# Performance work log

Measured on AMD Instinct MI355X. Metric: run time of the kernel, lower is better.

## Reference

```python
import jax, jax.numpy as jnp
import numpy as np

HEAD_SIZE = 128
LAMBDA_INIT = 0.8
FILL = 1e-09  # the module fills masked positions with 1e-9 (not -inf); reproduce faithfully


def setup_inputs() -> dict:
    key = jax.random.key(0)
    ks = jax.random.split(key, 12)
    B, T, C = 8, 2048, 1024
    q = jax.random.normal(ks[0], (B, T, C), dtype=jnp.float32)
    k = jax.random.normal(ks[1], (B, T, C), dtype=jnp.float32)
    v = jax.random.normal(ks[2], (B, T, C), dtype=jnp.float32)
    pad_mask = jax.random.randint(ks[3], (B, T), 0, 2, dtype=jnp.int32)
    scale = 1.0 / np.sqrt(C)
    Wq = jax.random.normal(ks[4], (C, 2 * HEAD_SIZE), dtype=jnp.float32) * scale
    Wk = jax.random.normal(ks[5], (C, 2 * HEAD_SIZE), dtype=jnp.float32) * scale
    Wv = jax.random.normal(ks[6], (C, HEAD_SIZE), dtype=jnp.float32) * scale
    lq1 = jax.random.normal(ks[7], (HEAD_SIZE,), dtype=jnp.float32)
    lk1 = jax.random.normal(ks[8], (HEAD_SIZE,), dtype=jnp.float32)
    lq2 = jax.random.normal(ks[9], (HEAD_SIZE,), dtype=jnp.float32)
    lk2 = jax.random.normal(ks[10], (HEAD_SIZE,), dtype=jnp.float32)
    return {"q": q, "k": k, "v": v, "pad_mask": pad_mask,
            "Wq": Wq, "Wk": Wk, "Wv": Wv,
            "lq1": lq1, "lk1": lk1, "lq2": lq2, "lk2": lk2}


def reference(q, k, v, pad_mask, Wq, Wk, Wv, lq1, lk1, lq2, lk2):
    B, T_q, C = q.shape
    T_k = k.shape[1]
    Q = q @ Wq                      # [B, Tq, 2*hs]
    K = k @ Wk                      # [B, Tk, 2*hs]
    V = v @ Wv                      # [B, Tk, ho]
    Q1, Q2 = jnp.split(Q, 2, axis=-1)
    K1, K2 = jnp.split(K, 2, axis=-1)
    s1 = jnp.einsum("bqd,bkd->bqk", Q1, K1)
    s2 = jnp.einsum("bqd,bkd->bqk", Q2, K2)
    # causal mask: tril(ones, diagonal=1) == 0 -> fill (note diagonal=1, one lookahead)
    causal_fill = jnp.tril(jnp.ones((T_q, T_k), dtype=bool), 1) == False
    s1 = jnp.where(causal_fill[None], FILL, s1)
    s2 = jnp.where(causal_fill[None], FILL, s2)
    # pad mask broadcast over the KEY axis per query row (as in original)
    pad_fill = (pad_mask == 1)[:, :, None]  # [B, Tq, 1]
    s1 = jnp.where(pad_fill, FILL, s1)
    s2 = jnp.where(pad_fill, FILL, s2)
    scale = HEAD_SIZE ** (-0.5)
    lbd = jnp.exp(jnp.dot(lq1, lk1)) - jnp.exp(jnp.dot(lq2, lk2)) + LAMBDA_INIT
    attn = jax.nn.softmax(s1 * scale, axis=-1) - lbd * jax.nn.softmax(s2 * scale, axis=-1)
    return attn @ V                 # [B, Tq, ho]
```

## Files before the change

kernel.cpp:

```cpp
#include <hip/hip_runtime.h>
#include <math.h>


#define T_SEQ 2048
#define NB 8
#define CDIM 1024
#define HS 128

constexpr float SCALE = 0.08838834764831845f;

typedef float f32x4 __attribute__((ext_vector_type(4)));
typedef __bf16 bf16x8 __attribute__((ext_vector_type(8)));
typedef unsigned int u32;

#define MFMA16 __builtin_amdgcn_mfma_f32_16x16x32_bf16

__device__ __forceinline__ void gld16(const void* g, void* l) {
  __builtin_amdgcn_global_load_lds(
      (const __attribute__((address_space(1))) u32*)g,
      (__attribute__((address_space(3))) u32*)l, 16, 0, 0);
}

__device__ __forceinline__ bf16x8 cvt8(f32x4 lo, f32x4 hi) {
  bf16x8 r;
  r[0] = (__bf16)lo.x; r[1] = (__bf16)lo.y; r[2] = (__bf16)lo.z; r[3] = (__bf16)lo.w;
  r[4] = (__bf16)hi.x; r[5] = (__bf16)hi.y; r[6] = (__bf16)hi.z; r[7] = (__bf16)hi.w;
  return r;
}

__global__ __launch_bounds__(128) void lambda_kernel(
    const float* __restrict__ lq1, const float* __restrict__ lk1,
    const float* __restrict__ lq2, const float* __restrict__ lk2,
    float* __restrict__ lbd) {
  __shared__ float r1[128], r2[128];
  int t = threadIdx.x;
  r1[t] = lq1[t] * lk1[t];
  r2[t] = lq2[t] * lk2[t];
  __syncthreads();
  for (int s = 64; s > 0; s >>= 1) {
    if (t < s) { r1[t] += r1[t + s]; r2[t] += r2[t + s]; }
    __syncthreads();
  }
  if (t == 0) *lbd = expf(r1[0]) - expf(r2[0]) + 0.8f;
}

__global__ __launch_bounds__(256) void pack_w(
    const float* __restrict__ Wq, const float* __restrict__ Wk,
    const float* __restrict__ Wv, __bf16* __restrict__ Wp) {
  int nt = blockIdx.x;
  const float* W; int colbase, N;
  if (nt < 16)      { W = Wq; colbase = nt * 16;        N = 256; }
  else if (nt < 32) { W = Wk; colbase = (nt - 16) * 16; N = 256; }
  else              { W = Wv; colbase = (nt - 32) * 16; N = 128; }
  int tid = threadIdx.x;
#pragma unroll
  for (int i = 0; i < 8; ++i) {
    int u = tid + 256 * i;
    int ks = u >> 6, lane = u & 63;
    int l15 = lane & 15, quad = lane >> 4;
    bf16x8 pk;
#pragma unroll
    for (int j = 0; j < 8; ++j)
      pk[j] = (__bf16)W[(size_t)(ks * 32 + quad * 8 + j) * N + colbase + l15];
    *(bf16x8*)(Wp + ((size_t)(nt * 32 + ks) * 64 + lane) * 8) = pk;
  }
}

template<int NT, int NTG>
__device__ __forceinline__ void proj_body(
    const float* __restrict__ Ablk, const __bf16* __restrict__ Wp,
    __bf16* __restrict__ outp, __bf16* __restrict__ Vt,
    int rows0, char* smem) {
  float*  sA = (float*)smem;
  __bf16* sB = (__bf16*)(smem + 32768);
  const int tid = threadIdx.x;
  const int lane = tid & 63, wave = tid >> 6;
  const int l15 = lane & 15, quad = lane >> 4;
  const int arow = lane >> 3;
  const int ac16 = (lane & 7) ^ arow;

  f32x4 acc0[NT], acc1[NT];
#pragma unroll
  for (int j = 0; j < NT; ++j) {
    acc0[j] = (f32x4){0.f, 0.f, 0.f, 0.f};
    acc1[j] = (f32x4){0.f, 0.f, 0.f, 0.f};
  }

  auto stage_ks = [&](int ks, int buf) {
    const float* gA = Ablk + ks * 32;
    float* lA = sA + buf * 4096;
#pragma unroll
    for (int i = 0; i < 4; ++i) {
      int li = wave * 4 + i;
      gld16(gA + (size_t)(li * 8 + arow) * CDIM + ac16 * 4, lA + li * 256);
    }
    __bf16* lB = sB + buf * 8192;
#pragma unroll
    for (int i = 0; i < 4; ++i) {
      int ntl = wave * 4 + i;
      if (ntl < NT)
        gld16(Wp + ((size_t)((NTG + ntl) * 32 + ks) * 64 + lane) * 8,
              lB + ntl * 512);
    }
  };

  stage_ks(0, 0);
  for (int ks = 0; ks < 32; ++ks) {
    const int buf = ks & 1;
    __syncthreads();
    const float* lA = sA + buf * 4096;
    int r0 = wave * 32 + l15;
    f32x4 lo0 = *(const f32x4*)(lA + r0 * 32 + (((quad * 2)     ^ (l15 & 7)) * 4));
    f32x4 hi0 = *(const f32x4*)(lA + r0 * 32 + (((quad * 2 + 1) ^ (l15 & 7)) * 4));
    bf16x8 af0 = cvt8(lo0, hi0);
    int r1 = r0 + 16;
    f32x4 lo1 = *(const f32x4*)(lA + r1 * 32 + (((quad * 2)     ^ (l15 & 7)) * 4));
    f32x4 hi1 = *(const f32x4*)(lA + r1 * 32 + (((quad * 2 + 1) ^ (l15 & 7)) * 4));
    bf16x8 af1 = cvt8(lo1, hi1);
    if (ks < 31) stage_ks(ks + 1, buf ^ 1);
    const __bf16* lB = sB + buf * 8192;
#pragma unroll
    for (int nt = 0; nt < NT; ++nt) {
      bf16x8 bf = *(const bf16x8*)(lB + nt * 512 + lane * 8);
      acc0[nt] = MFMA16(af0, bf, acc0[nt], 0, 0, 0);
      acc1[nt] = MFMA16(af1, bf, acc1[nt], 0, 0, 0);
    }
  }

  __syncthreads();
  __bf16* tile = (__bf16*)smem;
  constexpr int N = NT * 16;
#pragma unroll
  for (int half = 0; half < (NT >> 3); ++half) {
#pragma unroll
    for (int ntl = 0; ntl < 8; ++ntl) {
      f32x4 a0 = acc0[half * 8 + ntl];
      f32x4 a1 = acc1[half * 8 + ntl];
#pragma unroll
      for (int r = 0; r < 4; ++r) {
        tile[(wave * 32 + quad * 4 + r) * 136 + ntl * 16 + l15] = (__bf16)a0[r];
        tile[(wave * 32 + 16 + quad * 4 + r) * 136 + ntl * 16 + l15] = (__bf16)a1[r];
      }
    }
    __syncthreads();
#pragma unroll
    for (int i = 0; i < 8; ++i) {
      int u = tid + 256 * i;
      int row = u >> 4, c8 = u & 15;
      bf16x8 val = *(const bf16x8*)(tile + row * 136 + c8 * 8);
      *(bf16x8*)(outp + (size_t)(rows0 + row) * N + half * 128 + c8 * 8) = val;
    }
    if constexpr (NT == 8) {
      int b = rows0 >> 11, t0 = rows0 & 2047;
#pragma unroll
      for (int i = 0; i < 8; ++i) {
        int u = tid + 256 * i;
        int tc = u & 15, c = u >> 4;
        bf16x8 pk;
#pragma unroll
        for (int j = 0; j < 8; ++j) pk[j] = tile[(tc * 8 + j) * 136 + c];
        *(bf16x8*)(Vt + ((size_t)(b * 128 + c)) * T_SEQ + t0 + tc * 8) = pk;
      }
    }
    __syncthreads();
  }
}

__global__ __launch_bounds__(256, 2) void proj_mfma(
    const float* __restrict__ qin, const float* __restrict__ kin,
    const float* __restrict__ vin, const __bf16* __restrict__ Wp,
    __bf16* __restrict__ Qo, __bf16* __restrict__ Ko,
    __bf16* __restrict__ Vo, __bf16* __restrict__ Vt) {
  __shared__ char smem[65536];
  const int blk = blockIdx.x;
  const int rows0 = (blk & 127) * 128;
  if (blk < 128)
    proj_body<16, 0>(qin + (size_t)rows0 * CDIM, Wp, Qo, nullptr, rows0, smem);
  else if (blk < 256)
    proj_body<16, 16>(kin + (size_t)rows0 * CDIM, Wp, Ko, nullptr, rows0, smem);
  else
    proj_body<8, 32>(vin + (size_t)rows0 * CDIM, Wp, Vo, Vt, rows0, smem);
}

__global__ __launch_bounds__(128) void vcsum_a(const __bf16* __restrict__ V,
                                               float* __restrict__ csum) {
  int blk = blockIdx.x; int b = blk >> 4, ch = blk & 15;
  int c = threadIdx.x;
  const __bf16* vp = V + ((size_t)b * T_SEQ + ch * 128) * HS + c;
  float s = 0.f;
#pragma unroll 4
  for (int t = 0; t < 128; ++t) s += (float)vp[(size_t)t * HS];
  csum[(size_t)blk * HS + c] = s;
}

__global__ __launch_bounds__(128) void vcsum_b(const __bf16* __restrict__ V,
                                               const float* __restrict__ csum,
                                               float* __restrict__ cum) {
  int blk = blockIdx.x; int b = blk >> 4, ch = blk & 15;
  int c = threadIdx.x;
  float run = 0.f;
  for (int j = 0; j < ch; ++j) run += csum[(size_t)(b * 16 + j) * HS + c];
  const __bf16* vp = V + ((size_t)b * T_SEQ + ch * 128) * HS + c;
  float* cp = cum + ((size_t)b * (T_SEQ + 1) + ch * 128) * HS + c;
  if (ch == 0) cp[0] = 0.f;
#pragma unroll 4
  for (int t = 0; t < 128; ++t) {
    run += (float)vp[(size_t)t * HS];
    cp[(size_t)(t + 1) * HS] = run;
  }
}

__global__ __launch_bounds__(512, 2) void attn_mfma(
    const __bf16* __restrict__ Q, const __bf16* __restrict__ K,
    const __bf16* __restrict__ Vt, const float* __restrict__ cum,
    const int* __restrict__ pad, const float* __restrict__ lbdp,
    float* __restrict__ out) {
  __shared__ __bf16 sQ[32 * 264];
  __shared__ __bf16 sP[2][2][32 * 136];
  __shared__ float zb[2][32][64];
  __shared__ float zfin[2][32];

  const int tid = threadIdx.x;
  const int lane = tid & 63, wave = tid >> 6;
  const int wm = wave >> 2, wk = wave & 3;
  const int l15 = lane & 15, quad = lane >> 4;

  const int p = blockIdx.x;
  const int b = p & 7, q = p >> 3;
  const int ti = (q < 32) ? q : (95 - q);
  const int q0 = ti * 32;
  const float lbd = *lbdp;
  const __bf16* Qb = Q + (size_t)b * T_SEQ * 256;
  const __bf16* Kb = K + (size_t)b * T_SEQ * 256;
  const __bf16* Vtb = Vt + (size_t)b * HS * T_SEQ;
  const float* cumb = cum + (size_t)b * (T_SEQ + 1) * HS;
  const float pc = (1.f - lbd) * (1.f / (float)T_SEQ);

#pragma unroll
  for (int i = 0; i < 2; ++i) {
    int c = tid + 512 * i;
    int row = c >> 5, c16 = c & 31;
    *(f32x4*)(&sQ[row * 264 + c16 * 8]) =
        *(const f32x4*)(Qb + (size_t)(q0 + row) * 256 + c16 * 8);
  }
  __syncthreads();

  bf16x8 qf[2][4];
  {
    const int row = wm * 16 + l15;
#pragma unroll
    for (int pl = 0; pl < 2; ++pl)
#pragma unroll
      for (int s = 0; s < 4; ++s)
        qf[pl][s] = *(const bf16x8*)(&sQ[row * 264 + pl * 128 + s * 32 + quad * 8]);
  }

  f32x4 O[2][2];
#pragma unroll
  for (int i = 0; i < 2; ++i)
#pragma unroll
    for (int j = 0; j < 2; ++j) O[i][j] = (f32x4){0.f, 0.f, 0.f, 0.f};
  float z[2][4] = {};

  const int lastkey = q0 + 32;
  const int nkt = (min(lastkey, T_SEQ - 1) >> 7) + 1;

  for (int kt = 0; kt < nkt; ++kt) {
    const int k0 = kt << 7;
    const bool needmask = (k0 + 127 > q0 + 1);
    const int buf = kt & 1;

#pragma unroll
    for (int mat = 0; mat < 2; ++mat) {
      const __bf16* kp = Kb + (size_t)(k0 + wk * 32 + l15) * 256 + mat * 128 + quad * 8;
      bf16x8 ka0 = *(const bf16x8*)(kp);
      bf16x8 ka1 = *(const bf16x8*)(kp + 32);
      bf16x8 ka2 = *(const bf16x8*)(kp + 64);
      bf16x8 ka3 = *(const bf16x8*)(kp + 96);
      const __bf16* kq = kp + 16 * 256;
      bf16x8 kb0 = *(const bf16x8*)(kq);
      bf16x8 kb1 = *(const bf16x8*)(kq + 32);
      bf16x8 kb2 = *(const bf16x8*)(kq + 64);
      bf16x8 kb3 = *(const bf16x8*)(kq + 96);
      f32x4 S0 = (f32x4){0.f, 0.f, 0.f, 0.f}, S1 = S0;
      S0 = MFMA16(qf[mat][0], ka0, S0, 0, 0, 0);
      S0 = MFMA16(qf[mat][1], ka1, S0, 0, 0, 0);
      S0 = MFMA16(qf[mat][2], ka2, S0, 0, 0, 0);
      S0 = MFMA16(qf[mat][3], ka3, S0, 0, 0, 0);
      S1 = MFMA16(qf[mat][0], kb0, S1, 0, 0, 0);
      S1 = MFMA16(qf[mat][1], kb1, S1, 0, 0, 0);
      S1 = MFMA16(qf[mat][2], kb2, S1, 0, 0, 0);
      S1 = MFMA16(qf[mat][3], kb3, S1, 0, 0, 0);

      const int rowl = wm * 16 + quad * 4;
#pragma unroll
      for (int nt = 0; nt < 2; ++nt) {
        const int keyg = k0 + wk * 32 + nt * 16 + l15;
        const f32x4 Sv = nt ? S1 : S0;
#pragma unroll
        for (int r = 0; r < 4; ++r) {
          float pv;
          if (needmask) {
            int rowg = q0 + rowl + r;
            pv = (keyg <= rowg + 1) ? __expf(Sv[r] * SCALE) : 0.f;
          } else {
            pv = __expf(Sv[r] * SCALE);
          }
          z[mat][r] += pv;
          sP[buf][mat][(rowl + r) * 136 + wk * 32 + nt * 16 + l15] = (__bf16)pv;
        }
      }
    }
    __syncthreads();

#pragma unroll
    for (int ks = 0; ks < 4; ++ks) {
      bf16x8 pf0 = *(const bf16x8*)(&sP[buf][0][(wm * 16 + l15) * 136 + ks * 32 + quad * 8]);
      bf16x8 pf1 = *(const bf16x8*)(&sP[buf][1][(wm * 16 + l15) * 136 + ks * 32 + quad * 8]);
#pragma unroll
      for (int nt = 0; nt < 2; ++nt) {
        bf16x8 vf = *(const bf16x8*)(Vtb + (size_t)(wk * 32 + nt * 16 + l15) * T_SEQ +
                                     k0 + ks * 32 + quad * 8);
        O[0][nt] = MFMA16(pf0, vf, O[0][nt], 0, 0, 0);
        O[1][nt] = MFMA16(pf1, vf, O[1][nt], 0, 0, 0);
      }
    }
  }

#pragma unroll
  for (int mat = 0; mat < 2; ++mat)
#pragma unroll
    for (int r = 0; r < 4; ++r)
      zb[mat][wm * 16 + quad * 4 + r][wk * 16 + l15] = z[mat][r];
  __syncthreads();
  if (tid < 64) {
    int mat = tid >> 5, row = tid & 31;
    float s = 0.f;
#pragma unroll
    for (int j = 0; j < 64; ++j) s += zb[mat][row][(j + tid) & 63];
    zfin[mat][row] = s;
  }
  __syncthreads();

#pragma unroll
  for (int r = 0; r < 4; ++r) {
    const int rowl = wm * 16 + quad * 4 + r;
    const int rowg = q0 + rowl;
    const int nallow = min(rowg + 2, T_SEQ);
    const float nmask = (float)(T_SEQ - nallow);
    const float Z1 = zfin[0][rowl] + nmask;
    const float Z2 = zfin[1][rowl] + nmask;
    const float i1 = 1.f / Z1, i2 = lbd / Z2;
    const float tc = i1 - i2;
    const bool isp = (pad[b * T_SEQ + rowg] == 1);
#pragma unroll
    for (int nt = 0; nt < 2; ++nt) {
      const int col = wk * 32 + nt * 16 + l15;
      const float ct = cumb[(size_t)T_SEQ * HS + col];
      const float cn = cumb[(size_t)nallow * HS + col];
      float val = isp ? (pc * ct)
                      : (O[0][nt][r] * i1 - O[1][nt][r] * i2 + tc * (ct - cn));
      out[((size_t)b * T_SEQ + rowg) * HS + col] = val;
    }
  }
}

extern "C" void kernel_launch(void* const* d_in, const int* in_sizes, int n_in,
                              void* d_out, int out_size, void* d_ws, size_t ws_size,
                              hipStream_t stream) {
  (void)in_sizes; (void)n_in; (void)out_size; (void)ws_size;
  const float* q   = (const float*)d_in[0];
  const float* k   = (const float*)d_in[1];
  const float* v   = (const float*)d_in[2];
  const int*   pm  = (const int*)d_in[3];
  const float* Wq  = (const float*)d_in[4];
  const float* Wk  = (const float*)d_in[5];
  const float* Wv  = (const float*)d_in[6];
  const float* lq1 = (const float*)d_in[7];
  const float* lk1 = (const float*)d_in[8];
  const float* lq2 = (const float*)d_in[9];
  const float* lk2 = (const float*)d_in[10];
  float* out = (float*)d_out;
  char* ws = (char*)d_ws;

  float*  lbd  = (float*)ws;
  __bf16* Wp   = (__bf16*)(ws + 16);
  __bf16* Qp   = (__bf16*)(ws + 16 + 1310720);
  __bf16* Kp   = Qp + (size_t)NB * T_SEQ * 256;
  __bf16* Vp   = Kp + (size_t)NB * T_SEQ * 256;
  __bf16* Vt   = Vp + (size_t)NB * T_SEQ * HS;
  float*  cum  = (float*)(Vt + (size_t)NB * T_SEQ * HS);
  float*  csum = cum + (size_t)NB * (T_SEQ + 1) * HS;

  lambda_kernel<<<dim3(1), dim3(128), 0, stream>>>(lq1, lk1, lq2, lk2, lbd);
  pack_w<<<dim3(40), dim3(256), 0, stream>>>(Wq, Wk, Wv, Wp);
  proj_mfma<<<dim3(384), dim3(256), 0, stream>>>(q, k, v, Wp, Qp, Kp, Vp, Vt);
  vcsum_a<<<dim3(128), dim3(128), 0, stream>>>(Vp, csum);
  vcsum_b<<<dim3(128), dim3(128), 0, stream>>>(Vp, csum, cum);
  attn_mfma<<<dim3(512), dim3(512), 0, stream>>>(Qp, Kp, Vt, cum, pm, lbd, out);
}
```

Measured before the change: 379.4 us.

## Prefetch next K and V tiles into registers and schedule heaviest tiles first

Loads the K fragments for the next key tile right after the current QK^T MFMAs, and the V fragments right after the PV MFMAs, so global-load latency overlaps with the softmax and MFMA work instead of stalling each iteration. Also changes the block-to-query-tile mapping from a paired interleave to a plain descending order, so the longest causal rows are launched first. The cost is a larger register footprint (16 extra bf16x8 fragments per lane), which could cause spills under the 512-thread, 2-blocks-per-CU launch bound.

```diff
diff --git a/kernel.cpp b/kernel.cpp
--- a/kernel.cpp
+++ b/kernel.cpp
@@ -226,8 +226,8 @@
   const int l15 = lane & 15, quad = lane >> 4;
 
   const int p = blockIdx.x;
-  const int b = p & 7, q = p >> 3;
-  const int ti = (q < 32) ? q : (95 - q);
+  const int b = p & 7;
+  const int ti = 63 - (p >> 3);
   const int q0 = ti * 32;
   const float lbd = *lbdp;
   const __bf16* Qb = Q + (size_t)b * T_SEQ * 256;
@@ -236,6 +236,33 @@
   const float* cumb = cum + (size_t)b * (T_SEQ + 1) * HS;
   const float pc = (1.f - lbd) * (1.f / (float)T_SEQ);
 
+  const int lastkey = q0 + 32;
+  const int nkt = (min(lastkey, T_SEQ - 1) >> 7) + 1;
+
+  bf16x8 kf[2][2][4];
+  bf16x8 vf[2][4];
+  auto loadK = [&](int k0) {
+#pragma unroll
+    for (int mat = 0; mat < 2; ++mat) {
+      const __bf16* kp = Kb + (size_t)(k0 + wk * 32 + l15) * 256 + mat * 128 + quad * 8;
+#pragma unroll
+      for (int s = 0; s < 4; ++s) {
+        kf[mat][0][s] = *(const bf16x8*)(kp + s * 32);
+        kf[mat][1][s] = *(const bf16x8*)(kp + 16 * 256 + s * 32);
+      }
+    }
+  };
+  auto loadV = [&](int k0) {
+#pragma unroll
+    for (int nt = 0; nt < 2; ++nt)
+#pragma unroll
+      for (int ks = 0; ks < 4; ++ks)
+        vf[nt][ks] = *(const bf16x8*)(Vtb + (size_t)(wk * 32 + nt * 16 + l15) * T_SEQ +
+                                      k0 + ks * 32 + quad * 8);
+  };
+  loadK(0);
+  loadV(0);
+
 #pragma unroll
   for (int i = 0; i < 2; ++i) {
     int c = tid + 512 * i;
@@ -262,55 +289,43 @@
     for (int j = 0; j < 2; ++j) O[i][j] = (f32x4){0.f, 0.f, 0.f, 0.f};
   float z[2][4] = {};
 
-  const int lastkey = q0 + 32;
-  const int nkt = (min(lastkey, T_SEQ - 1) >> 7) + 1;
-
   for (int kt = 0; kt < nkt; ++kt) {
     const int k0 = kt << 7;
     const bool needmask = (k0 + 127 > q0 + 1);
     const int buf = kt & 1;
 
+    f32x4 S[2][2];
 #pragma unroll
     for (int mat = 0; mat < 2; ++mat) {
-      const __bf16* kp = Kb + (size_t)(k0 + wk * 32 + l15) * 256 + mat * 128 + quad * 8;
-      bf16x8 ka0 = *(const bf16x8*)(kp);
-      bf16x8 ka1 = *(const bf16x8*)(kp + 32);
-      bf16x8 ka2 = *(const bf16x8*)(kp + 64);
-      bf16x8 ka3 = *(const bf16x8*)(kp + 96);
-      const __bf16* kq = kp + 16 * 256;
-      bf16x8 kb0 = *(const bf16x8*)(kq);
-      bf16x8 kb1 = *(const bf16x8*)(kq + 32);
-      bf16x8 kb2 = *(const bf16x8*)(kq + 64);
-      bf16x8 kb3 = *(const bf16x8*)(kq + 96);
-      f32x4 S0 = (f32x4){0.f, 0.f, 0.f, 0.f}, S1 = S0;
-      S0 = MFMA16(qf[mat][0], ka0, S0, 0, 0, 0);
-      S0 = MFMA16(qf[mat][1], ka1, S0, 0, 0, 0);
-      S0 = MFMA16(qf[mat][2], ka2, S0, 0, 0, 0);
-      S0 = MFMA16(qf[mat][3], ka3, S0, 0, 0, 0);
-      S1 = MFMA16(qf[mat][0], kb0, S1, 0, 0, 0);
-      S1 = MFMA16(qf[mat][1], kb1, S1, 0, 0, 0);
-      S1 = MFMA16(qf[mat][2], kb2, S1, 0, 0, 0);
-      S1 = MFMA16(qf[mat][3], kb3, S1, 0, 0, 0);
-
-      const int rowl = wm * 16 + quad * 4;
+      S[mat][0] = (f32x4){0.f, 0.f, 0.f, 0.f};
+      S[mat][1] = (f32x4){0.f, 0.f, 0.f, 0.f};
+#pragma unroll
+      for (int s = 0; s < 4; ++s) {
+        S[mat][0] = MFMA16(qf[mat][s], kf[mat][0][s], S[mat][0], 0, 0, 0);
+        S[mat][1] = MFMA16(qf[mat][s], kf[mat][1][s], S[mat][1], 0, 0, 0);
+      }
+    }
+    if (kt + 1 < nkt) loadK(k0 + 128);
+
+    const int rowl = wm * 16 + quad * 4;
+#pragma unroll
+    for (int mat = 0; mat < 2; ++mat)
 #pragma unroll
       for (int nt = 0; nt < 2; ++nt) {
         const int keyg = k0 + wk * 32 + nt * 16 + l15;
-        const f32x4 Sv = nt ? S1 : S0;
 #pragma unroll
         for (int r = 0; r < 4; ++r) {
           float pv;
           if (needmask) {
             int rowg = q0 + rowl + r;
-            pv = (keyg <= rowg + 1) ? __expf(Sv[r] * SCALE) : 0.f;
+            pv = (keyg <= rowg + 1) ? __expf(S[mat][nt][r] * SCALE) : 0.f;
           } else {
-            pv = __expf(Sv[r] * SCALE);
+            pv = __expf(S[mat][nt][r] * SCALE);
           }
           z[mat][r] += pv;
           sP[buf][mat][(rowl + r) * 136 + wk * 32 + nt * 16 + l15] = (__bf16)pv;
         }
       }
-    }
     __syncthreads();
 
 #pragma unroll
@@ -319,12 +334,11 @@
       bf16x8 pf1 = *(const bf16x8*)(&sP[buf][1][(wm * 16 + l15) * 136 + ks * 32 + quad * 8]);
 #pragma unroll
       for (int nt = 0; nt < 2; ++nt) {
-        bf16x8 vf = *(const bf16x8*)(Vtb + (size_t)(wk * 32 + nt * 16 + l15) * T_SEQ +
-                                     k0 + ks * 32 + quad * 8);
-        O[0][nt] = MFMA16(pf0, vf, O[0][nt], 0, 0, 0);
-        O[1][nt] = MFMA16(pf1, vf, O[1][nt], 0, 0, 0);
-      }
-    }
+        O[0][nt] = MFMA16(pf0, vf[nt][ks], O[0][nt], 0, 0, 0);
+        O[1][nt] = MFMA16(pf1, vf[nt][ks], O[1][nt], 0, 0, 0);
+      }
+    }
+    if (kt + 1 < nkt) loadV(k0 + 128);
   }
 
 #pragma unroll
```

After: 373.9 us. No clear change (-1.5%).
